# Kernel tuning notes

Hardware: AMD Instinct MI355X
Metric: run time of the kernel (lower is better)

Reference implementation:

```python
import jax, jax.numpy as jnp
import numpy as np

DIM = 512
H = 48
W = 48
WS = 6
NH = 16
HEAD = DIM // NH
SCALE = HEAD ** -0.5
MLP_RATIO = 4
EPS = 1e-3  # keras LayerNormalization default epsilon
B = 16
L = H * W
M = WS * WS
NW = (H // WS) * (W // WS)


def _rel_pos_index(ws):
    # replicates tf.meshgrid (indexing='xy') construction exactly
    ch = np.arange(ws)
    cw = np.arange(ws)
    coords = np.stack(np.meshgrid(ch, cw))              # (2, ws, ws)
    cf = coords.reshape(2, -1)                          # (2, M)
    cf1 = np.concatenate([cf, np.zeros((2, 1), cf.dtype)], axis=1)  # (2, M+1) with global (0,0)
    rel = cf[:, :, None] - cf1[:, None, :]              # (2, M, M+1)
    rel = rel.transpose(1, 2, 0).copy()
    rel[:, :, 0] += ws - 1
    rel[:, :, 1] += ws - 1
    rel[:, :, 0] *= 2 * ws - 1
    return rel.sum(-1)                                  # (M, M+1)

REL_IDX = jnp.asarray(_rel_pos_index(WS))


def layernorm(x, g, b):
    m = x.mean(-1, keepdims=True)
    v = ((x - m) ** 2).mean(-1, keepdims=True)
    return (x - m) / jnp.sqrt(v + EPS) * g + b


def setup_inputs() -> dict:
    key = jax.random.key(0)
    ks = jax.random.split(key, 8)
    dense = lambda k, i, o: jax.random.normal(k, (i, o), jnp.float32) * (1.0 / np.sqrt(i))
    return dict(
        x=jax.random.normal(ks[0], (B, L, DIM), jnp.float32),
        xavg=jax.random.normal(ks[1], (B, 1, DIM), jnp.float32),
        w_kv=dense(ks[2], DIM, 2 * DIM), b_kv=jnp.zeros((2 * DIM,), jnp.float32),
        w_q=dense(ks[3], DIM, DIM), b_q=jnp.zeros((DIM,), jnp.float32),
        rel_bias_table=jax.random.normal(ks[4], ((2 * WS - 1) ** 2, NH), jnp.float32) * 0.02,
        g1=jnp.ones((DIM,), jnp.float32), be1=jnp.zeros((DIM,), jnp.float32),
        g2=jnp.ones((DIM,), jnp.float32), be2=jnp.zeros((DIM,), jnp.float32),
        w_fc1=dense(ks[5], DIM, MLP_RATIO * DIM), b_fc1=jnp.zeros((MLP_RATIO * DIM,), jnp.float32),
        w_fc2=dense(ks[6], MLP_RATIO * DIM, DIM), b_fc2=jnp.zeros((DIM,), jnp.float32),
    )


def _heads(t):
    # (B*, N, C) -> (B*, NH, N, HEAD)
    return t.reshape(t.shape[0], t.shape[1], NH, HEAD).transpose(0, 2, 1, 3)


def _forward(x, xavg, w_kv, b_kv, w_q, b_q, rel_bias_table, g1, be1, g2, be2,
             w_fc1, b_fc1, w_fc2, b_fc2):
    shortcut, shortcut_avg = x, xavg
    xn = layernorm(x, g1, be1)                          # (B, L, C)
    xavgn = layernorm(xavg, g1, be1)                    # (B, 1, C)

    # window partition: (B, L, C) -> (B*NW, M, C)
    xw = xn.reshape(B, H // WS, WS, W // WS, WS, DIM)
    xw = xw.transpose(0, 1, 3, 2, 4, 5).reshape(B * NW, M, DIM)

    # per-window tokens + repeated global token as keys/values
    xavgR = jnp.repeat(xavgn, NW, axis=0)               # (B*NW, 1, C), batch-major like tf.repeat
    x_c = jnp.concatenate([xw, xavgR], axis=1)          # (B*NW, M+1, C)

    kv = x_c @ w_kv + b_kv                              # (B*NW, M+1, 2C)
    q = xw @ w_q + b_q                                  # (B*NW, M, C)
    q_avg = xavgn @ w_q + b_q                           # (B, 1, C)
    kv_g = xn @ w_kv + b_kv                             # (B, L, 2C)

    k, v = jnp.split(kv, 2, axis=-1)
    kg, vg = jnp.split(kv_g, 2, axis=-1)

    qh = _heads(q) * SCALE                              # (B*NW, NH, M, HEAD)
    attn = jnp.einsum('bhqd,bhkd->bhqk', qh, _heads(k))  # (B*NW, NH, M, M+1)
    bias = rel_bias_table[REL_IDX.reshape(-1)].reshape(M, M + 1, NH)
    attn = attn + bias.transpose(2, 0, 1)[None]
    attn = jax.nn.softmax(attn, axis=-1)
    xo = jnp.einsum('bhqk,bhkd->bhqd', attn, _heads(v))
    xo = xo.transpose(0, 2, 1, 3).reshape(B * NW, M, DIM)

    # global token attends to all tokens
    qg = _heads(q_avg) * SCALE                          # (B, NH, 1, HEAD)
    attng = jax.nn.softmax(jnp.einsum('bhqd,bhkd->bhqk', qg, _heads(kg)), axis=-1)
    xavg_o = jnp.einsum('bhqk,bhkd->bhqd', attng, _heads(vg))
    xavg_o = xavg_o.transpose(0, 2, 1, 3).reshape(B, 1, DIM)

    # window reverse: (B*NW, M, C) -> (B, L, C)
    xr = xo.reshape(B, H // WS, W // WS, WS, WS, DIM)
    xr = xr.transpose(0, 1, 3, 2, 4, 5).reshape(B, L, DIM)

    x = shortcut + xr
    xavg = shortcut_avg + xavg_o

    mlp = lambda t: jax.nn.gelu(t @ w_fc1 + b_fc1, approximate=False) @ w_fc2 + b_fc2
    x = x + mlp(layernorm(x, g2, be2))
    xavg = xavg + mlp(layernorm(xavg, g2, be2))
    return x, xavg


def reference(x, xavg, w_kv, b_kv, w_q, b_q, rel_bias_table, g1, be1, g2, be2,
              w_fc1, b_fc1, w_fc2, b_fc2):
    return _forward(x, xavg, w_kv, b_kv, w_q, b_q, rel_bias_table, g1, be1, g2, be2,
                    w_fc1, b_fc1, w_fc2, b_fc2)
```

## Files before the change

### kernel.cpp

```cpp
#include <hip/hip_runtime.h>
#include <stdint.h>

#define DIM 512
#define NHEAD 16
#define HEADD 32
#define BATCH 16
#define SEQL 2304
#define XROWS (BATCH*SEQL)
#define NROWS (XROWS + BATCH)
#define ATT_SCALE 0.17677669529663687f

typedef __attribute__((ext_vector_type(8))) short short8;
typedef __attribute__((ext_vector_type(4))) float f32x4;

__device__ __forceinline__ float bf2f(unsigned short v) {
    union { unsigned u; float f; } t; t.u = ((unsigned)v) << 16; return t.f;
}
__device__ __forceinline__ unsigned short f2bf(float f) {
    union { float f; unsigned u; } t; t.f = f;
    unsigned r = t.u + 0x7fffu + ((t.u >> 16) & 1u);
    return (unsigned short)(r >> 16);
}
__device__ __forceinline__ void unpack8(const int4 c, float* o) {
    union { unsigned u; float f; } t;
    unsigned w0 = (unsigned)c.x, w1 = (unsigned)c.y, w2 = (unsigned)c.z, w3 = (unsigned)c.w;
    t.u = w0 << 16;         o[0] = t.f;
    t.u = w0 & 0xffff0000u; o[1] = t.f;
    t.u = w1 << 16;         o[2] = t.f;
    t.u = w1 & 0xffff0000u; o[3] = t.f;
    t.u = w2 << 16;         o[4] = t.f;
    t.u = w2 & 0xffff0000u; o[5] = t.f;
    t.u = w3 << 16;         o[6] = t.f;
    t.u = w3 & 0xffff0000u; o[7] = t.f;
}
__device__ __forceinline__ void gl_lds16(const void* g, void* l) {
    __builtin_amdgcn_global_load_lds((const __attribute__((address_space(1))) unsigned int*)g,
                                     (__attribute__((address_space(3))) unsigned int*)l,
                                     16, 0, 0);
}

__device__ __forceinline__ float gelu_exact(float v) {
    union { float f; unsigned u; } zc; zc.f = v * 0.70710678118654752f;
    unsigned sgn = zc.u & 0x80000000u;
    union { float f; unsigned u; } az; az.u = zc.u & 0x7fffffffu;
    float t  = __builtin_amdgcn_rcpf(fmaf(0.3275911f, az.f, 1.0f));
    float p  = t * fmaf(t, fmaf(t, fmaf(t, fmaf(t, 1.061405429f, -1.453152027f),
                                        1.421413741f), -0.284496736f), 0.254829592f);
    float e  = __expf(-az.f * az.f);
    union { float f; unsigned u; } er; er.f = fmaf(-p, e, 1.0f);
    er.u |= sgn;
    return 0.5f * v * (1.0f + er.f);
}

__global__ __launch_bounds__(256) void tpose_kernel(const float* __restrict__ w_q,
                                                    const float* __restrict__ w_kv,
                                                    const float* __restrict__ w_fc1,
                                                    const float* __restrict__ w_fc2,
                                                    unsigned short* __restrict__ Wqkv_t,
                                                    unsigned short* __restrict__ Wfc1_t,
                                                    unsigned short* __restrict__ Wfc2_t) {
    __shared__ float tile[32][33];
    int t = blockIdx.x;
    const float* src; unsigned short* dst;
    int Kd, Nd, rowOff, tk;
    if (t < 256)        { src = w_q;   dst = Wqkv_t; Kd = 512;  Nd = 512;  rowOff = 0;   tk = 16; }
    else if (t < 768)   { t -= 256;  src = w_kv;  dst = Wqkv_t; Kd = 512;  Nd = 1024; rowOff = 512; tk = 16; }
    else if (t < 1792)  { t -= 768;  src = w_fc1; dst = Wfc1_t; Kd = 512;  Nd = 2048; rowOff = 0;   tk = 16; }
    else                { t -= 1792; src = w_fc2; dst = Wfc2_t; Kd = 2048; Nd = 512;  rowOff = 0;   tk = 64; }
    int k0 = (t % tk) * 32;
    int n0 = (t / tk) * 32;
    int tx = threadIdx.x & 31, ty = threadIdx.x >> 5;
    #pragma unroll
    for (int r = 0; r < 32; r += 8)
        tile[r + ty][tx] = src[(long)(k0 + r + ty) * Nd + n0 + tx];
    __syncthreads();
    #pragma unroll
    for (int r = 0; r < 32; r += 8)
        dst[(long)(rowOff + n0 + r + ty) * Kd + k0 + tx] = f2bf(tile[tx][r + ty]);
}

__global__ void smallpack_kernel(const float* __restrict__ b_q, const float* __restrict__ b_kv,
                                 const float* __restrict__ rel_table,
                                 float* __restrict__ bqkv, float* __restrict__ bias_exp) {
    int i = blockIdx.x * 256 + threadIdx.x;
    if (i < 1536) { bqkv[i] = (i < 512) ? b_q[i] : b_kv[i - 512]; return; }
    i -= 1536;
    if (i < NHEAD*36*37) {
        int h = i / (36*37); int rem = i % (36*37); int qi = rem / 37; int j = rem % 37;
        int c0m = qi % 6, c1m = qi / 6;
        int c0n = (j < 36) ? (j % 6) : 0;
        int c1n = (j < 36) ? (j / 6) : 0;
        int id = (c0m - c0n + 5) * 11 + (c1m - c1n + 5);
        bias_exp[i] = rel_table[id * NHEAD + h];
    }
}

__global__ __launch_bounds__(256) void ln_kernel(const float* __restrict__ p1,
                                                 const float* __restrict__ p2, int split,
                                                 const float* __restrict__ g, const float* __restrict__ be,
                                                 unsigned short* __restrict__ out, int nrows) {
    int wv = threadIdx.x >> 6, lane = threadIdx.x & 63;
    int r = blockIdx.x * 4 + wv;
    if (r >= nrows) return;
    const float* src = (r < split) ? (p1 + (long)r * DIM) : (p2 + (long)(r - split) * DIM);
    int c0 = lane * 8;
    float4 v0 = *(const float4*)(src + c0);
    float4 v1 = *(const float4*)(src + c0 + 4);
    float s = v0.x+v0.y+v0.z+v0.w + v1.x+v1.y+v1.z+v1.w;
    float q = v0.x*v0.x+v0.y*v0.y+v0.z*v0.z+v0.w*v0.w + v1.x*v1.x+v1.y*v1.y+v1.z*v1.z+v1.w*v1.w;
    for (int m = 1; m < 64; m <<= 1) { s += __shfl_xor(s, m); q += __shfl_xor(q, m); }
    float mean = s * (1.0f/512.0f);
    float var  = q * (1.0f/512.0f) - mean*mean;
    float rs = rsqrtf(var + 1e-3f);
    float4 g0 = *(const float4*)(g + c0);
    float4 g1 = *(const float4*)(g + c0 + 4);
    float4 b0 = *(const float4*)(be + c0);
    float4 b1 = *(const float4*)(be + c0 + 4);
    unsigned short o[8];
    o[0] = f2bf((v0.x-mean)*rs*g0.x + b0.x);
    o[1] = f2bf((v0.y-mean)*rs*g0.y + b0.y);
    o[2] = f2bf((v0.z-mean)*rs*g0.z + b0.z);
    o[3] = f2bf((v0.w-mean)*rs*g0.w + b0.w);
    o[4] = f2bf((v1.x-mean)*rs*g1.x + b1.x);
    o[5] = f2bf((v1.y-mean)*rs*g1.y + b1.y);
    o[6] = f2bf((v1.z-mean)*rs*g1.z + b1.z);
    o[7] = f2bf((v1.w-mean)*rs*g1.w + b1.w);
    *(int4*)(out + (long)r * DIM + c0) = *(const int4*)o;
}

template<bool GELU_ACT, bool OUT_BF16, bool HAS_RES>
__global__ __launch_bounds__(256) void gemm_kernel(const short* __restrict__ A,
                                                   const short* __restrict__ Bt,
                                                   const float* __restrict__ bias,
                                                   void* __restrict__ Cout,
                                                   const float* __restrict__ Res,
                                                   int M, int N, int K) {
    __shared__ short lds_a[128 * 64];
    __shared__ short lds_b[128 * 64];
    const int tid = threadIdx.x;
    const int lane = tid & 63;
    const int wv = tid >> 6;
    const int m0 = blockIdx.y * 128;
    const int n0 = blockIdx.x * 128;
    const int wm = (wv >> 1) * 64;
    const int wn = (wv & 1) * 64;

    f32x4 acc[4][4];
    #pragma unroll
    for (int i = 0; i < 4; i++)
        #pragma unroll
        for (int j = 0; j < 4; j++) { acc[i][j][0]=0.f; acc[i][j][1]=0.f; acc[i][j][2]=0.f; acc[i][j][3]=0.f; }

    const int srow = tid >> 3;
    const int ssl  = tid & 7;
    const int msl  = ssl ^ (srow & 7);
    const short* Aa = A + (long)(m0 + srow) * K + msl * 8;
    const short* Bb = Bt + (long)(n0 + srow) * K + msl * 8;
    short* la = lds_a + tid * 8;
    short* lb = lds_b + tid * 8;

    const int quad = lane >> 4;
    const int l15 = lane & 15;
    const short* ra0 = lds_a + (wm + l15) * 64 + ((quad)     ^ (l15 & 7)) * 8;
    const short* ra1 = lds_a + (wm + l15) * 64 + ((4 + quad) ^ (l15 & 7)) * 8;
    const short* rb0 = lds_b + (wn + l15) * 64 + ((quad)     ^ (l15 & 7)) * 8;
    const short* rb1 = lds_b + (wn + l15) * 64 + ((4 + quad) ^ (l15 & 7)) * 8;

    for (int k0 = 0; k0 < K; k0 += 64) {
        __syncthreads();
        #pragma unroll
        for (int i = 0; i < 4; i++) {
            gl_lds16(Aa + (long)(i * 32) * K + k0, la + i * 256 * 8);
            gl_lds16(Bb + (long)(i * 32) * K + k0, lb + i * 256 * 8);
        }
        __syncthreads();
        short8 af[4], bf[4];
        #pragma unroll
        for (int mt = 0; mt < 4; mt++) af[mt] = *(const short8*)(ra0 + mt * 16 * 64);
        #pragma unroll
        for (int nt = 0; nt < 4; nt++) bf[nt] = *(const short8*)(rb0 + nt * 16 * 64);
        #pragma unroll
        for (int mt = 0; mt < 4; mt++)
            #pragma unroll
            for (int nt = 0; nt < 4; nt++)
                acc[mt][nt] = __builtin_amdgcn_mfma_f32_16x16x32_bf16(af[mt], bf[nt], acc[mt][nt], 0, 0, 0);
        #pragma unroll
        for (int mt = 0; mt < 4; mt++) af[mt] = *(const short8*)(ra1 + mt * 16 * 64);
        #pragma unroll
        for (int nt = 0; nt < 4; nt++) bf[nt] = *(const short8*)(rb1 + nt * 16 * 64);
        #pragma unroll
        for (int mt = 0; mt < 4; mt++)
            #pragma unroll
            for (int nt = 0; nt < 4; nt++)
                acc[mt][nt] = __builtin_amdgcn_mfma_f32_16x16x32_bf16(af[mt], bf[nt], acc[mt][nt], 0, 0, 0);
    }

    #pragma unroll
    for (int mt = 0; mt < 4; mt++) {
        int rbase = m0 + wm + mt * 16 + quad * 4;
        #pragma unroll
        for (int nt = 0; nt < 4; nt++) {
            int col = n0 + wn + nt * 16 + l15;
            float bv = bias[col];
            #pragma unroll
            for (int r = 0; r < 4; r++) {
                int row = rbase + r;
                if (row < M) {
                    float v = acc[mt][nt][r] + bv;
                    if (GELU_ACT) v = gelu_exact(v);
                    if (HAS_RES) v += Res[(long)row * N + col];
                    if (OUT_BF16) ((unsigned short*)Cout)[(long)row * N + col] = f2bf(v);
                    else          ((float*)Cout)[(long)row * N + col] = v;
                }
            }
        }
    }
}

__global__ __launch_bounds__(256) void winattn_kernel(const short* __restrict__ qkv,
                                                      const float* __restrict__ bias_exp,
                                                      const float* __restrict__ xin,
                                                      float* __restrict__ XALL) {
    __shared__ float kvs[4][37 * 64];
    const int tid = threadIdx.x;
    const int wv = tid >> 6;
    const int lane = tid & 63;
    const int gw = blockIdx.x * 4 + wv;
    const int win = gw >> 4;
    const int h = gw & 15;
    const int b = win >> 6;
    const int i1 = (win >> 3) & 7;
    const int i3 = win & 7;

    float* lws = kvs[wv];

    for (int c = lane; c < 296; c += 64) {
        int cc = c;
        int voff = 512;
        int doff = 0;
        if (cc >= 148) { cc -= 148; voff = 1024; doff = 32; }
        int row = cc >> 2;
        int part = cc & 3;
        int grow;
        if (row < 36) { int i2 = row / 6, i4 = row % 6; grow = b * SEQL + (i1*6 + i2) * 48 + i3*6 + i4; }
        else grow = XROWS + b;
        int4 raw = *(const int4*)(qkv + (long)grow * 1536 + voff + h * 32 + part * 8);
        float tmp[8];
        unpack8(raw, tmp);
        float* dstp = &lws[row * 64 + doff + part * 8];
        *(float4*)dstp       = make_float4(tmp[0], tmp[1], tmp[2], tmp[3]);
        *(float4*)(dstp + 4) = make_float4(tmp[4], tmp[5], tmp[6], tmp[7]);
    }
    __syncthreads();

    const int qi = lane;
    if (qi >= 36) return;
    int i2 = qi / 6, i4 = qi % 6;
    const int growq = b * SEQL + (i1*6 + i2) * 48 + i3*6 + i4;

    float qr[32];
    {
        const int4* qp = (const int4*)(qkv + (long)growq * 1536 + h * 32);
        unpack8(qp[0], qr); unpack8(qp[1], qr + 8); unpack8(qp[2], qr + 16); unpack8(qp[3], qr + 24);
        #pragma unroll
        for (int d = 0; d < 32; d++) qr[d] *= ATT_SCALE;
    }

    const float* brow = bias_exp + h * (36*37) + qi * 37;
    float s[37];
    float mx = -1e30f;
    #pragma unroll
    for (int j = 0; j < 37; j++) {
        float kr[32];
        #pragma unroll
        for (int t4 = 0; t4 < 8; t4++) *(float4*)(kr + t4*4) = *(const float4*)(lws + j * 64 + t4 * 4);
        float d0 = 0.f, d1 = 0.f, d2 = 0.f, d3 = 0.f;
        #pragma unroll
        for (int dd = 0; dd < 8; dd++) {
            d0 += qr[dd]      * kr[dd];
            d1 += qr[8 + dd]  * kr[8 + dd];
            d2 += qr[16 + dd] * kr[16 + dd];
            d3 += qr[24 + dd] * kr[24 + dd];
        }
        float sv = (d0 + d1 + d2 + d3) + brow[j];
        s[j] = sv;
        mx = fmaxf(mx, sv);
    }
    float sum = 0.f;
    #pragma unroll
    for (int j = 0; j < 37; j++) { s[j] = __expf(s[j] - mx); sum += s[j]; }
    float inv_sum = 1.0f / sum;

    float o[32];
    #pragma unroll
    for (int dd = 0; dd < 32; dd++) o[dd] = 0.f;
    #pragma unroll
    for (int j = 0; j < 37; j++) {
        float vr[32];
        #pragma unroll
        for (int t4 = 0; t4 < 8; t4++) *(float4*)(vr + t4*4) = *(const float4*)(lws + j * 64 + 32 + t4 * 4);
        float p = s[j];
        #pragma unroll
        for (int dd = 0; dd < 32; dd++) o[dd] += p * vr[dd];
    }

    const float* xi = xin + (long)growq * DIM + h * 32;
    float* xo = XALL + (long)growq * DIM + h * 32;
    #pragma unroll
    for (int v4 = 0; v4 < 8; v4++) {
        float4 xv = *(const float4*)(xi + v4 * 4);
        float4 ov;
        ov.x = xv.x + o[v4*4 + 0] * inv_sum;
        ov.y = xv.y + o[v4*4 + 1] * inv_sum;
        ov.z = xv.z + o[v4*4 + 2] * inv_sum;
        ov.w = xv.w + o[v4*4 + 3] * inv_sum;
        *(float4*)(xo + v4 * 4) = ov;
    }
}

__global__ __launch_bounds__(256) void gattn_kernel(const short* __restrict__ qkv,
                                                    const float* __restrict__ xavg,
                                                    float* __restrict__ XALL) {
    const int b = blockIdx.x >> 4;
    const int h = blockIdx.x & 15;
    const int tid = threadIdx.x;
    __shared__ float qs[32];
    __shared__ float redm[4], redsum[4];
    __shared__ float wout[4][32];
    if (tid < 32) qs[tid] = bf2f(((const unsigned short*)qkv)[(long)(XROWS + b) * 1536 + h * 32 + tid]);
    __syncthreads();
    float qr[32];
    #pragma unroll
    for (int d = 0; d < 32; d++) qr[d] = qs[d];
    float s[9];
    float mx = -1e30f;
    #pragma unroll
    for (int i = 0; i < 9; i++) {
        int t = tid + i * 256;
        const int4* kp = (const int4*)(qkv + (long)(b * SEQL + t) * 1536 + 512 + h * 32);
        float kr[32];
        unpack8(kp[0], kr); unpack8(kp[1], kr + 8); unpack8(kp[2], kr + 16); unpack8(kp[3], kr + 24);
        float d0 = 0.f, d1 = 0.f, d2 = 0.f, d3 = 0.f;
        #pragma unroll
        for (int dd = 0; dd < 8; dd++) {
            d0 += qr[dd] * kr[dd]; d1 += qr[8+dd] * kr[8+dd];
            d2 += qr[16+dd] * kr[16+dd]; d3 += qr[24+dd] * kr[24+dd];
        }
        s[i] = (d0 + d1 + d2 + d3) * ATT_SCALE;
        mx = fmaxf(mx, s[i]);
    }
    for (int m = 1; m < 64; m <<= 1) mx = fmaxf(mx, __shfl_xor(mx, m));
    if ((tid & 63) == 0) redm[tid >> 6] = mx;
    __syncthreads();
    mx = fmaxf(fmaxf(redm[0], redm[1]), fmaxf(redm[2], redm[3]));
    float sum = 0.f;
    #pragma unroll
    for (int i = 0; i < 9; i++) { s[i] = __expf(s[i] - mx); sum += s[i]; }
    for (int m = 1; m < 64; m <<= 1) sum += __shfl_xor(sum, m);
    if ((tid & 63) == 0) redsum[tid >> 6] = sum;
    __syncthreads();
    sum = redsum[0] + redsum[1] + redsum[2] + redsum[3];
    float o[32];
    #pragma unroll
    for (int d = 0; d < 32; d++) o[d] = 0.f;
    #pragma unroll
    for (int i = 0; i < 9; i++) {
        int t = tid + i * 256;
        const int4* vp = (const int4*)(qkv + (long)(b * SEQL + t) * 1536 + 1024 + h * 32);
        float vr[32];
        unpack8(vp[0], vr); unpack8(vp[1], vr + 8); unpack8(vp[2], vr + 16); unpack8(vp[3], vr + 24);
        float p = s[i];
        #pragma unroll
        for (int d = 0; d < 32; d++) o[d] += p * vr[d];
    }
    for (int m = 1; m < 64; m <<= 1) {
        #pragma unroll
        for (int d = 0; d < 32; d++) o[d] += __shfl_xor(o[d], m);
    }
    if ((tid & 63) == 0) {
        #pragma unroll
        for (int d = 0; d < 32; d++) wout[tid >> 6][d] = o[d];
    }
    __syncthreads();
    if (tid < 32) {
        float t = wout[0][tid] + wout[1][tid] + wout[2][tid] + wout[3][tid];
        XALL[(long)(XROWS + b) * DIM + h * 32 + tid] = xavg[b * DIM + h * 32 + tid] + t / sum;
    }
}

extern "C" void kernel_launch(void* const* d_in, const int* in_sizes, int n_in,
                              void* d_out, int out_size, void* d_ws, size_t ws_size,
                              hipStream_t stream) {
    const float* x      = (const float*)d_in[0];
    const float* xavg   = (const float*)d_in[1];
    const float* w_kv   = (const float*)d_in[2];
    const float* b_kv   = (const float*)d_in[3];
    const float* w_q    = (const float*)d_in[4];
    const float* b_q    = (const float*)d_in[5];
    const float* rel    = (const float*)d_in[6];
    const float* g1     = (const float*)d_in[7];
    const float* be1    = (const float*)d_in[8];
    const float* g2     = (const float*)d_in[9];
    const float* be2    = (const float*)d_in[10];
    const float* w_fc1  = (const float*)d_in[11];
    const float* b_fc1  = (const float*)d_in[12];
    const float* w_fc2  = (const float*)d_in[13];
    const float* b_fc2  = (const float*)d_in[14];

    char* ws = (char*)d_ws;
    size_t off = 0;
    auto alloc = [&](size_t bytes) { void* p = ws + off; off += (bytes + 255) & ~(size_t)255; return p; };
    short* qkv_h          = (short*)alloc((size_t)NROWS * 2048 * 2);
    float* XALL           = (float*)alloc((size_t)NROWS * 512 * 4);
    short* xn             = (short*)alloc((size_t)NROWS * 512 * 2);
    unsigned short* Wqkv_t = (unsigned short*)alloc((size_t)1536 * 512 * 2);
    unsigned short* Wfc1_t = (unsigned short*)alloc((size_t)2048 * 512 * 2);
    unsigned short* Wfc2_t = (unsigned short*)alloc((size_t)512 * 2048 * 2);
    float* bqkv           = (float*)alloc(1536 * 4);
    float* bias_exp       = (float*)alloc((size_t)NHEAD * 36 * 37 * 4);

    tpose_kernel<<<2816, 256, 0, stream>>>(w_q, w_kv, w_fc1, w_fc2,
                                           Wqkv_t, Wfc1_t, Wfc2_t);
    smallpack_kernel<<<(1536 + NHEAD*36*37 + 255) / 256, 256, 0, stream>>>(b_q, b_kv, rel, bqkv, bias_exp);
    ln_kernel<<<(NROWS + 3) / 4, 256, 0, stream>>>(x, xavg, XROWS, g1, be1, (unsigned short*)xn, NROWS);
    gemm_kernel<false, true, false><<<dim3(1536 / 128, (NROWS + 127) / 128), 256, 0, stream>>>(
        xn, (const short*)Wqkv_t, bqkv, qkv_h, nullptr, NROWS, 1536, 512);
    winattn_kernel<<<1024 * 16 / 4, 256, 0, stream>>>(qkv_h, bias_exp, x, XALL);
    gattn_kernel<<<256, 256, 0, stream>>>(qkv_h, xavg, XALL);
    ln_kernel<<<(NROWS + 3) / 4, 256, 0, stream>>>(XALL, XALL + (size_t)XROWS * 512, XROWS, g2, be2,
                                                   (unsigned short*)xn, NROWS);
    gemm_kernel<true, true, false><<<dim3(2048 / 128, (NROWS + 127) / 128), 256, 0, stream>>>(
        xn, (const short*)Wfc1_t, b_fc1, qkv_h, nullptr, NROWS, 2048, 512);
    gemm_kernel<false, false, true><<<dim3(512 / 128, (NROWS + 127) / 128), 256, 0, stream>>>(
        qkv_h, (const short*)Wfc2_t, b_fc2, d_out, XALL, NROWS, 512, 2048);
}
```

Before: 732.4 us.

## Double-buffer GEMM LDS tiles and remap workgroups across XCDs

The GEMM kernel now uses two LDS buffers and issues the global-to-LDS loads for the next K tile before computing the current one. It waits with s_waitcnt vmcnt and raw barriers, so memory latency overlaps with MFMA work. The launch also switches to a 1D grid with an XCD-aware block remap, so consecutive tiles land on the same XCD and share L2. The cost is double the LDS footprint, which can lower occupancy, and hand-written waitcnt assumptions that could break if the compiler reorders loads.

```diff
diff --git a/kernel.cpp b/kernel.cpp
--- a/kernel.cpp
+++ b/kernel.cpp
@@ -134,14 +134,20 @@
                                                    const float* __restrict__ bias,
                                                    void* __restrict__ Cout,
                                                    const float* __restrict__ Res,
-                                                   int M, int N, int K) {
-    __shared__ short lds_a[128 * 64];
-    __shared__ short lds_b[128 * 64];
+                                                   int M, int N, int K, int nbx) {
+    __shared__ short lds_a[2][128 * 64];
+    __shared__ short lds_b[2][128 * 64];
     const int tid = threadIdx.x;
     const int lane = tid & 63;
     const int wv = tid >> 6;
-    const int m0 = blockIdx.y * 128;
-    const int n0 = blockIdx.x * 128;
+
+    const int nwg = gridDim.x;
+    const int orig = blockIdx.x;
+    const int q = nwg >> 3, r = nwg & 7;
+    const int xcd = orig & 7, lid = orig >> 3;
+    const int wg = (xcd < r ? xcd * (q + 1) : r * (q + 1) + (xcd - r) * q) + lid;
+    const int m0 = (wg / nbx) * 128;
+    const int n0 = (wg % nbx) * 128;
     const int wm = (wv >> 1) * 64;
     const int wn = (wv & 1) * 64;
 
@@ -152,47 +158,62 @@
         for (int j = 0; j < 4; j++) { acc[i][j][0]=0.f; acc[i][j][1]=0.f; acc[i][j][2]=0.f; acc[i][j][3]=0.f; }
 
     const int srow = tid >> 3;
-    const int ssl  = tid & 7;
-    const int msl  = ssl ^ (srow & 7);
+    const int msl  = (tid & 7) ^ (srow & 7);
     const short* Aa = A + (long)(m0 + srow) * K + msl * 8;
     const short* Bb = Bt + (long)(n0 + srow) * K + msl * 8;
-    short* la = lds_a + tid * 8;
-    short* lb = lds_b + tid * 8;
 
     const int quad = lane >> 4;
     const int l15 = lane & 15;
-    const short* ra0 = lds_a + (wm + l15) * 64 + ((quad)     ^ (l15 & 7)) * 8;
-    const short* ra1 = lds_a + (wm + l15) * 64 + ((4 + quad) ^ (l15 & 7)) * 8;
-    const short* rb0 = lds_b + (wn + l15) * 64 + ((quad)     ^ (l15 & 7)) * 8;
-    const short* rb1 = lds_b + (wn + l15) * 64 + ((4 + quad) ^ (l15 & 7)) * 8;
-
+    const int ro_a0 = (wm + l15) * 64 + ((quad)     ^ (l15 & 7)) * 8;
+    const int ro_a1 = (wm + l15) * 64 + ((4 + quad) ^ (l15 & 7)) * 8;
+    const int ro_b0 = (wn + l15) * 64 + ((quad)     ^ (l15 & 7)) * 8;
+    const int ro_b1 = (wn + l15) * 64 + ((4 + quad) ^ (l15 & 7)) * 8;
+
+    auto stage = [&](int buf, int k0) {
+        short* la = &lds_a[buf][tid * 8];
+        short* lb = &lds_b[buf][tid * 8];
+        #pragma unroll
+        for (int i = 0; i < 4; i++) {
+            gl_lds16(Aa + (long)(i * 32) * K + k0, la + i * 2048);
+            gl_lds16(Bb + (long)(i * 32) * K + k0, lb + i * 2048);
+        }
+    };
+
+    stage(0, 0);
+    int cur = 0;
     for (int k0 = 0; k0 < K; k0 += 64) {
-        __syncthreads();
-        #pragma unroll
-        for (int i = 0; i < 4; i++) {
-            gl_lds16(Aa + (long)(i * 32) * K + k0, la + i * 256 * 8);
-            gl_lds16(Bb + (long)(i * 32) * K + k0, lb + i * 256 * 8);
+        if (k0 + 64 < K) {
+            stage(cur ^ 1, k0 + 64);
+            asm volatile("s_waitcnt vmcnt(8)" ::: "memory");
+        } else {
+            asm volatile("s_waitcnt vmcnt(0)" ::: "memory");
         }
-        __syncthreads();
-        short8 af[4], bf[4];
-        #pragma unroll
-        for (int mt = 0; mt < 4; mt++) af[mt] = *(const short8*)(ra0 + mt * 16 * 64);
-        #pragma unroll
-        for (int nt = 0; nt < 4; nt++) bf[nt] = *(const short8*)(rb0 + nt * 16 * 64);
+        __builtin_amdgcn_s_barrier();
+        asm volatile("" ::: "memory");
+        const short* ba = lds_a[cur];
+        const short* bb = lds_b[cur];
+        short8 af[4], bf4[4];
+        #pragma unroll
+        for (int mt = 0; mt < 4; mt++) af[mt] = *(const short8*)(ba + ro_a0 + mt * 1024);
+        #pragma unroll
+        for (int nt = 0; nt < 4; nt++) bf4[nt] = *(const short8*)(bb + ro_b0 + nt * 1024);
         #pragma unroll
         for (int mt = 0; mt < 4; mt++)
             #pragma unroll
             for (int nt = 0; nt < 4; nt++)
-                acc[mt][nt] = __builtin_amdgcn_mfma_f32_16x16x32_bf16(af[mt], bf[nt], acc[mt][nt], 0, 0, 0);
-        #pragma unroll
-        for (int mt = 0; mt < 4; mt++) af[mt] = *(const short8*)(ra1 + mt * 16 * 64);
-        #pragma unroll
-        for (int nt = 0; nt < 4; nt++) bf[nt] = *(const short8*)(rb1 + nt * 16 * 64);
+                acc[mt][nt] = __builtin_amdgcn_mfma_f32_16x16x32_bf16(af[mt], bf4[nt], acc[mt][nt], 0, 0, 0);
+        #pragma unroll
+        for (int mt = 0; mt < 4; mt++) af[mt] = *(const short8*)(ba + ro_a1 + mt * 1024);
+        #pragma unroll
+        for (int nt = 0; nt < 4; nt++) bf4[nt] = *(const short8*)(bb + ro_b1 + nt * 1024);
         #pragma unroll
         for (int mt = 0; mt < 4; mt++)
             #pragma unroll
             for (int nt = 0; nt < 4; nt++)
-                acc[mt][nt] = __builtin_amdgcn_mfma_f32_16x16x32_bf16(af[mt], bf[nt], acc[mt][nt], 0, 0, 0);
+                acc[mt][nt] = __builtin_amdgcn_mfma_f32_16x16x32_bf16(af[mt], bf4[nt], acc[mt][nt], 0, 0, 0);
+        asm volatile("" ::: "memory");
+        __builtin_amdgcn_s_barrier();
+        cur ^= 1;
     }
 
     #pragma unroll
@@ -203,10 +224,10 @@
             int col = n0 + wn + nt * 16 + l15;
             float bv = bias[col];
             #pragma unroll
-            for (int r = 0; r < 4; r++) {
-                int row = rbase + r;
+            for (int r2 = 0; r2 < 4; r2++) {
+                int row = rbase + r2;
                 if (row < M) {
-                    float v = acc[mt][nt][r] + bv;
+                    float v = acc[mt][nt][r2] + bv;
                     if (GELU_ACT) v = gelu_exact(v);
                     if (HAS_RES) v += Res[(long)row * N + col];
                     if (OUT_BF16) ((unsigned short*)Cout)[(long)row * N + col] = f2bf(v);
@@ -419,18 +440,20 @@
     float* bqkv           = (float*)alloc(1536 * 4);
     float* bias_exp       = (float*)alloc((size_t)NHEAD * 36 * 37 * 4);
 
+    const int MB = (NROWS + 127) / 128;
+
     tpose_kernel<<<2816, 256, 0, stream>>>(w_q, w_kv, w_fc1, w_fc2,
                                            Wqkv_t, Wfc1_t, Wfc2_t);
     smallpack_kernel<<<(1536 + NHEAD*36*37 + 255) / 256, 256, 0, stream>>>(b_q, b_kv, rel, bqkv, bias_exp);
     ln_kernel<<<(NROWS + 3) / 4, 256, 0, stream>>>(x, xavg, XROWS, g1, be1, (unsigned short*)xn, NROWS);
-    gemm_kernel<false, true, false><<<dim3(1536 / 128, (NROWS + 127) / 128), 256, 0, stream>>>(
-        xn, (const short*)Wqkv_t, bqkv, qkv_h, nullptr, NROWS, 1536, 512);
+    gemm_kernel<false, true, false><<<12 * MB, 256, 0, stream>>>(
+        xn, (const short*)Wqkv_t, bqkv, qkv_h, nullptr, NROWS, 1536, 512, 12);
     winattn_kernel<<<1024 * 16 / 4, 256, 0, stream>>>(qkv_h, bias_exp, x, XALL);
     gattn_kernel<<<256, 256, 0, stream>>>(qkv_h, xavg, XALL);
     ln_kernel<<<(NROWS + 3) / 4, 256, 0, stream>>>(XALL, XALL + (size_t)XROWS * 512, XROWS, g2, be2,
                                                    (unsigned short*)xn, NROWS);
-    gemm_kernel<true, true, false><<<dim3(2048 / 128, (NROWS + 127) / 128), 256, 0, stream>>>(
-        xn, (const short*)Wfc1_t, b_fc1, qkv_h, nullptr, NROWS, 2048, 512);
-    gemm_kernel<false, false, true><<<dim3(512 / 128, (NROWS + 127) / 128), 256, 0, stream>>>(
-        qkv_h, (const short*)Wfc2_t, b_fc2, d_out, XALL, NROWS, 512, 2048);
-}
+    gemm_kernel<true, true, false><<<16 * MB, 256, 0, stream>>>(
+        xn, (const short*)Wfc1_t, b_fc1, qkv_h, nullptr, NROWS, 2048, 512, 16);
+    gemm_kernel<false, false, true><<<4 * MB, 256, 0, stream>>>(
+        qkv_h, (const short*)Wfc2_t, b_fc2, d_out, XALL, NROWS, 512, 2048, 4);
+}
```

Result: slower. 849.9 us (+16.0%).
